# Optimization experiments

Hardware: AMD Instinct MI355X
Metric: run time of the kernel (lower is better)

## Reference

```python
import jax, jax.numpy as jnp
import numpy as np

B, S, H, HD = 8, 1024, 16, 64
D = H * HD
NINF = -10000.0
EPS = 1e-6


def setup_inputs() -> dict:
    key = jax.random.key(0)
    ks = jax.random.split(key, 6)
    std = 0.02
    return {
        "x": jax.random.normal(ks[0], (B, S, D), jnp.float32),
        "mask": jax.random.randint(ks[1], (B, S), 0, 2, jnp.int32),
        "wq": jax.random.normal(ks[2], (D, D), jnp.float32) * std,
        "bq": jnp.zeros((D,), jnp.float32),
        "wk": jax.random.normal(ks[3], (D, D), jnp.float32) * std,
        "bk": jnp.zeros((D,), jnp.float32),
        "wv": jax.random.normal(ks[4], (D, D), jnp.float32) * std,
        "bv": jnp.zeros((D,), jnp.float32),
        "wo": jax.random.normal(ks[5], (D, D), jnp.float32) * std,
        "bo": jnp.zeros((D,), jnp.float32),
        "gamma": jnp.ones((D,), jnp.float32),
        "beta": jnp.zeros((D,), jnp.float32),
    }


def _heads(t):
    # [B,S,D] -> [B,H,S,HD]
    return t.reshape(t.shape[0], t.shape[1], H, HD).transpose(0, 2, 1, 3)


def _layernorm(x, gamma, beta):
    mu = jnp.mean(x, -1, keepdims=True)
    var = jnp.mean(jnp.square(x - mu), -1, keepdims=True)
    return (x - mu) * jax.lax.rsqrt(var + EPS) * gamma + beta


def reference(x, mask, wq, bq, wk, bk, wv, bv, wo, bo, gamma, beta):
    q = _heads(x @ wq + bq)
    k = _heads(x @ wk + bk)
    v = _heads(x @ wv + bv)
    scores = jnp.einsum("bhqd,bhkd->bhqk", q, k) / np.sqrt(HD).astype(np.float32)
    # padding mask broadcast over key axis: 1 = masked
    scores = scores + mask.astype(jnp.float32)[:, None, None, :] * NINF
    attn = jax.nn.softmax(scores, axis=-1)
    ctx = jnp.einsum("bhqk,bhkd->bhqd", attn, v)  # [B,H,S,HD]
    ctx = ctx.transpose(0, 2, 1, 3).reshape(B, S, D)
    out = _layernorm(x + ctx @ wo + bo, gamma, beta)
    return out
```

## Files before the change

### kernel.cpp

```cpp
#include <hip/hip_runtime.h>
#include <stdint.h>

typedef unsigned short u16;
typedef unsigned int u32;
typedef __bf16 b16x8 __attribute__((ext_vector_type(8)));
typedef float f32x4 __attribute__((ext_vector_type(4)));

#define B_ 8
#define S_ 1024
#define H_ 16
#define HD_ 64
#define D_ 1024
#define M_ 8192

__device__ __forceinline__ u16 f2bf(float f) {
  u32 u = __float_as_uint(f);
  return (u16)((u + 0x7fffu + ((u >> 16) & 1u)) >> 16);
}
__device__ __forceinline__ u16 bfbits(float f) {
  union {
    __bf16 b;
    u16 u;
  } c;
  c.b = (__bf16)f;
  return c.u;
}

__device__ __forceinline__ f32x4 mfma16(b16x8 a, b16x8 b, f32x4 c) {
  return __builtin_amdgcn_mfma_f32_16x16x32_bf16(a, b, c, 0, 0, 0);
}

__device__ __forceinline__ void cp16(const u16* g, u16* l) {
  __builtin_amdgcn_global_load_lds(
      (const __attribute__((address_space(1))) u32*)(g),
      (__attribute__((address_space(3))) u32*)(l), 16, 0, 0);
}

__global__ __launch_bounds__(1024) void wconv_kernel(
    const float* __restrict__ w0, const float* __restrict__ w1,
    const float* __restrict__ w2, const float* __restrict__ w3,
    u16* __restrict__ t0, u16* __restrict__ t1, u16* __restrict__ t2,
    u16* __restrict__ t3) {
  __shared__ float tile[32][33];
  const int z = blockIdx.z;
  const float* src = (z == 0) ? w0 : (z == 1) ? w1 : (z == 2) ? w2 : w3;
  u16* dst = (z == 0) ? t0 : (z == 1) ? t1 : (z == 2) ? t2 : t3;
  const int tx = threadIdx.x, ty = threadIdx.y;
  const int x0 = blockIdx.x * 32, y0 = blockIdx.y * 32;
  tile[ty][tx] = src[(size_t)(y0 + ty) * D_ + x0 + tx];
  __syncthreads();
  dst[(size_t)(x0 + ty) * D_ + y0 + tx] = f2bf(tile[tx][ty]);
}

__global__ __launch_bounds__(256) void xconv_kernel(const float* __restrict__ x,
                                                    u16* __restrict__ xb) {
  const size_t i = ((size_t)blockIdx.x * 256 + threadIdx.x) * 4;
  const float4 v = *(const float4*)(x + i);
  u16 o[4] = {f2bf(v.x), f2bf(v.y), f2bf(v.z), f2bf(v.w)};
  uint2 pack;
  pack.x = ((u32)o[1] << 16) | o[0];
  pack.y = ((u32)o[3] << 16) | o[2];
  *(uint2*)(xb + i) = pack;
}

#define ABUF_ 16384
#define BBUF_ 8192
#define BUFSZ_ (ABUF_ + BBUF_)

__device__ __forceinline__ void gemm256x128_mainloop(
    const u16* __restrict__ A, const u16* __restrict__ BT, int K, int m0,
    int n0, u16* lds, f32x4 (&acc)[4][4]) {
  const int t = threadIdx.x;
  const int lane = t & 63;
  const int l15 = lane & 15;
  const int q4 = lane >> 4;
  const int w = t >> 6;
  const int wm = w >> 1;
  const int wn = w & 1;

  const f32x4 zero = {0.f, 0.f, 0.f, 0.f};
#pragma unroll
  for (int mt = 0; mt < 4; ++mt)
#pragma unroll
    for (int nt = 0; nt < 4; ++nt) acc[mt][nt] = zero;

  const int rbase = t >> 3;
  const int scol = ((t & 7) ^ (rbase & 7)) * 8;
  const u16* Ag = A + (size_t)(m0 + rbase) * K + scol;
  const u16* Bg = BT + (size_t)(n0 + rbase) * K + scol;
  const int sx = l15 & 7;

  auto STAGE = [&](int kt, int bufi) {
    u16* Ab = lds + bufi * BUFSZ_;
    u16* Bb = Ab + ABUF_;
    const int k0 = kt * 64;
#pragma unroll
    for (int c = 0; c < 4; ++c)
      cp16(Ag + (size_t)(c * 64) * K + k0, Ab + c * 4096 + t * 8);
#pragma unroll
    for (int c = 0; c < 2; ++c)
      cp16(Bg + (size_t)(c * 64) * K + k0, Bb + c * 4096 + t * 8);
  };

  const int NT = K / 64;
  STAGE(0, 0);
  STAGE(1, 1);

  int cur = 0;
  for (int kt = 0; kt < NT; ++kt) {
    if (kt + 2 < NT) {
      int nb = cur + 2;
      if (nb >= 3) nb -= 3;
      STAGE(kt + 2, nb);
    }
    if (kt + 2 < NT)
      asm volatile("s_waitcnt vmcnt(12)" ::: "memory");
    else if (kt + 1 < NT)
      asm volatile("s_waitcnt vmcnt(6)" ::: "memory");
    else
      asm volatile("s_waitcnt vmcnt(0)" ::: "memory");
    asm volatile("s_barrier" ::: "memory");

    const u16* Ab = lds + cur * BUFSZ_;
    const u16* Bb = Ab + ABUF_;

    b16x8 af[4][2], bf2[4][2];
#pragma unroll
    for (int kk = 0; kk < 2; ++kk) {
      const int cc = ((kk * 4 + q4) ^ sx) * 8;
#pragma unroll
      for (int mt = 0; mt < 4; ++mt)
        af[mt][kk] = *(const b16x8*)(Ab + (wm * 64 + mt * 16 + l15) * 64 + cc);
#pragma unroll
      for (int nt = 0; nt < 4; ++nt)
        bf2[nt][kk] = *(const b16x8*)(Bb + (wn * 64 + nt * 16 + l15) * 64 + cc);
    }
    __builtin_amdgcn_sched_barrier(0);

    __builtin_amdgcn_s_setprio(1);
#pragma unroll
    for (int mt = 0; mt < 4; ++mt)
#pragma unroll
      for (int nt = 0; nt < 4; ++nt)
        acc[mt][nt] = mfma16(af[mt][0], bf2[nt][0], acc[mt][nt]);
    __builtin_amdgcn_s_setprio(0);

    asm volatile("s_waitcnt lgkmcnt(0)" ::: "memory");
    asm volatile("s_barrier" ::: "memory");

    __builtin_amdgcn_s_setprio(1);
#pragma unroll
    for (int mt = 0; mt < 4; ++mt)
#pragma unroll
      for (int nt = 0; nt < 4; ++nt)
        acc[mt][nt] = mfma16(af[mt][1], bf2[nt][1], acc[mt][nt]);
    __builtin_amdgcn_s_setprio(0);

    ++cur;
    if (cur == 3) cur = 0;
  }
}

__global__ __launch_bounds__(512, 2) void qkv_gemm_kernel(
    const u16* __restrict__ xb, const u16* __restrict__ wt3,
    const float* __restrict__ bq, const float* __restrict__ bk,
    const float* __restrict__ bv, u16* __restrict__ Q, u16* __restrict__ Kb,
    u16* __restrict__ VT) {
  __shared__ __align__(16) u16 lds[3 * BUFSZ_];
  const int wg = blockIdx.x;
  const int xcd = wg & 7;
  const int s = wg >> 3;
  const int by = xcd * 4 + (s & 3);
  const int bx = s >> 2;
  const int m0 = by * 256;
  const int n0 = bx * 128;

  f32x4 acc[4][4];
  gemm256x128_mainloop(xb, wt3, D_, m0, n0, lds, acc);

  const int t = threadIdx.x;
  const int lane = t & 63, w = t >> 6;
  const int l15 = lane & 15, q4 = lane >> 4;
  const int wm = w >> 1, wn = w & 1;

  const int z = n0 >> 10;
  u16* out = (z == 0) ? Q : (z == 1) ? Kb : VT;
  const float* bias = (z == 0) ? bq : (z == 1) ? bk : bv;

  for (int nt = 0; nt < 4; ++nt) {
    const int nf = n0 + wn * 64 + nt * 16 + l15;
    const int n1 = nf & 1023;
    const float bias_v = bias[n1];
    const int h = n1 >> 6, hd = n1 & 63;
    for (int mt = 0; mt < 4; ++mt) {
      for (int r = 0; r < 4; ++r) {
        const int m = m0 + wm * 64 + mt * 16 + q4 * 4 + r;
        const int b = m >> 10, ss = m & 1023;
        const float v = acc[mt][nt][r] + bias_v;
        size_t idx;
        if (z < 2)
          idx = (((size_t)(b * H_ + h)) * S_ + ss) * HD_ + hd;
        else
          idx = (((size_t)(b * H_ + h)) * HD_ + hd) * S_ + ss;
        out[idx] = f2bf(v);
      }
    }
  }
}

#define PAD_ 68
#define QPAD_ 72
__global__ __launch_bounds__(512) void attn_kernel(
    const u16* __restrict__ Q, const u16* __restrict__ Kb,
    const u16* __restrict__ VT, const int* __restrict__ mask,
    u16* __restrict__ ctx) {
  __shared__ __align__(16) u16 QPlds[128 * QPAD_];
  __shared__ __align__(16) u16 Klds[64 * PAD_];
  __shared__ __align__(16) u16 Vlds[64 * PAD_];
  __shared__ __align__(16) float Mlds[1024];

  const int t = threadIdx.x;
  const int lane = t & 63, w = t >> 6;
  const int l15 = lane & 15, q4 = lane >> 4;
  const int id = blockIdx.x;
  const int bh = id & 127;
  const int b = bh >> 4, h = bh & 15;
  const int q0 = (id >> 7) * 128;

  const u16* Qbh = Q + (size_t)bh * S_ * HD_;
  const u16* Kbh = Kb + (size_t)bh * S_ * HD_;
  const u16* Vbh = VT + (size_t)bh * S_ * HD_;
  const int* maskb = mask + b * S_;

  const int srow = t >> 3, scol = (t & 7) * 8;
  {
    b16x8 q0v = *(const b16x8*)(Qbh + (size_t)(q0 + srow) * HD_ + scol);
    b16x8 q1v = *(const b16x8*)(Qbh + (size_t)(q0 + srow + 64) * HD_ + scol);
    const int2 mv = *(const int2*)(maskb + t * 2);
    *(b16x8*)(QPlds + srow * QPAD_ + scol) = q0v;
    *(b16x8*)(QPlds + (srow + 64) * QPAD_ + scol) = q1v;
    float2 mf;
    mf.x = -14427.0f * (float)mv.x;
    mf.y = -14427.0f * (float)mv.y;
    *(float2*)(Mlds + t * 2) = mf;
  }
  __syncthreads();
  b16x8 aq[2];
  aq[0] = *(const b16x8*)(QPlds + (w * 16 + l15) * QPAD_ + q4 * 8);
  aq[1] = *(const b16x8*)(QPlds + (w * 16 + l15) * QPAD_ + 32 + q4 * 8);

  const f32x4 zero = {0.f, 0.f, 0.f, 0.f};
  f32x4 acc[4];
  for (int nt = 0; nt < 4; ++nt) acc[nt] = zero;
  float lsum = 0.f;
  u16* Pw = QPlds + w * 16 * QPAD_;
  const float c1 = 0.18033688f;

  b16x8 kv0 = *(const b16x8*)(Kbh + (size_t)srow * HD_ + scol);
  b16x8 vv0 = *(const b16x8*)(Vbh + (size_t)srow * S_ + scol);

  for (int j = 0; j < 16; ++j) {
    const int key0 = j * 64;
    __syncthreads();
    *(b16x8*)(Klds + srow * PAD_ + scol) = kv0;
    *(b16x8*)(Vlds + srow * PAD_ + scol) = vv0;
    __syncthreads();

    if (j < 15) {
      const int kn = key0 + 64;
      kv0 = *(const b16x8*)(Kbh + (size_t)(kn + srow) * HD_ + scol);
      vv0 = *(const b16x8*)(Vbh + (size_t)srow * S_ + kn + scol);
    }

    f32x4 sf[4];
    for (int nt = 0; nt < 4; ++nt) sf[nt] = zero;
    for (int kk = 0; kk < 2; ++kk)
      for (int nt = 0; nt < 4; ++nt) {
        b16x8 bk =
            *(const b16x8*)(Klds + (nt * 16 + l15) * PAD_ + kk * 32 + q4 * 8);
        sf[nt] = mfma16(bk, aq[kk], sf[nt]);
      }

    for (int nt = 0; nt < 4; ++nt) {
      const float4 mk = *(const float4*)(Mlds + key0 + nt * 16 + q4 * 4);
      float p0 = __builtin_amdgcn_exp2f(sf[nt][0] * c1 + mk.x);
      float p1 = __builtin_amdgcn_exp2f(sf[nt][1] * c1 + mk.y);
      float p2 = __builtin_amdgcn_exp2f(sf[nt][2] * c1 + mk.z);
      float p3 = __builtin_amdgcn_exp2f(sf[nt][3] * c1 + mk.w);
      lsum += (p0 + p1) + (p2 + p3);
      uint2 pk;
      pk.x = ((u32)bfbits(p1) << 16) | bfbits(p0);
      pk.y = ((u32)bfbits(p3) << 16) | bfbits(p2);
      *(uint2*)(Pw + l15 * QPAD_ + nt * 16 + q4 * 4) = pk;
    }
    asm volatile("s_waitcnt lgkmcnt(0)" ::: "memory");

    for (int kk = 0; kk < 2; ++kk) {
      b16x8 bp = *(const b16x8*)(Pw + l15 * QPAD_ + kk * 32 + q4 * 8);
      for (int nt = 0; nt < 4; ++nt) {
        b16x8 vb =
            *(const b16x8*)(Vlds + (nt * 16 + l15) * PAD_ + kk * 32 + q4 * 8);
        acc[nt] = mfma16(vb, bp, acc[nt]);
      }
    }
  }

  lsum += __shfl_xor(lsum, 16);
  lsum += __shfl_xor(lsum, 32);
  const float inv = 1.0f / lsum;

  const int srw = q0 + w * 16 + l15;
  u16* crow = ctx + ((size_t)(b * S_ + srw)) * D_ + h * 64;
  for (int nt = 0; nt < 4; ++nt) {
    uint2 pk;
    pk.x = ((u32)bfbits(acc[nt][1] * inv) << 16) | bfbits(acc[nt][0] * inv);
    pk.y = ((u32)bfbits(acc[nt][3] * inv) << 16) | bfbits(acc[nt][2] * inv);
    *(uint2*)(crow + nt * 16 + q4 * 4) = pk;
  }
}

__global__ __launch_bounds__(512, 2) void out_gemm_kernel(
    const u16* __restrict__ ctx, const u16* __restrict__ wto,
    const float* __restrict__ bo, const float* __restrict__ x,
    float* __restrict__ y) {
  __shared__ __align__(16) u16 lds[3 * BUFSZ_];
  const int wg = blockIdx.x;
  const int xcd = wg & 7;
  const int s = wg >> 3;
  const int by = xcd * 4 + (s & 3);
  const int bx = s >> 2;
  const int m0 = by * 256, n0 = bx * 128;

  f32x4 acc[4][4];
  gemm256x128_mainloop(ctx, wto, D_, m0, n0, lds, acc);

  const int t = threadIdx.x;
  const int lane = t & 63, w = t >> 6;
  const int l15 = lane & 15, q4 = lane >> 4;
  const int wm = w >> 1, wn = w & 1;

  for (int nt = 0; nt < 4; ++nt) {
    const int n = n0 + wn * 64 + nt * 16 + l15;
    const float bias = bo[n];
    for (int mt = 0; mt < 4; ++mt) {
      for (int r = 0; r < 4; ++r) {
        const int m = m0 + wm * 64 + mt * 16 + q4 * 4 + r;
        y[(size_t)m * D_ + n] = acc[mt][nt][r] + bias + x[(size_t)m * D_ + n];
      }
    }
  }
}

__global__ __launch_bounds__(256) void ln_kernel(const float* __restrict__ y,
                                                 const float* __restrict__ g,
                                                 const float* __restrict__ be,
                                                 float* __restrict__ out) {
  const int row = blockIdx.x, t = threadIdx.x;
  const float* yr = y + (size_t)row * D_;
  const float4 v = *(const float4*)(yr + t * 4);
  float s = v.x + v.y + v.z + v.w;
  float ss = v.x * v.x + v.y * v.y + v.z * v.z + v.w * v.w;
  for (int off = 1; off < 64; off <<= 1) {
    s += __shfl_xor(s, off);
    ss += __shfl_xor(ss, off);
  }
  __shared__ float red[8];
  const int w = t >> 6, lane = t & 63;
  if (lane == 0) {
    red[w] = s;
    red[4 + w] = ss;
  }
  __syncthreads();
  s = red[0] + red[1] + red[2] + red[3];
  ss = red[4] + red[5] + red[6] + red[7];
  const float mu = s * (1.f / 1024.f);
  const float var = ss * (1.f / 1024.f) - mu * mu;
  const float rs = rsqrtf(var + 1e-6f);
  const int c = t * 4;
  const float4 gv = *(const float4*)(g + c);
  const float4 bv = *(const float4*)(be + c);
  float4 o;
  o.x = (v.x - mu) * rs * gv.x + bv.x;
  o.y = (v.y - mu) * rs * gv.y + bv.y;
  o.z = (v.z - mu) * rs * gv.z + bv.z;
  o.w = (v.w - mu) * rs * gv.w + bv.w;
  *(float4*)(out + (size_t)row * D_ + c) = o;
}

extern "C" void kernel_launch(void* const* d_in, const int* in_sizes, int n_in,
                              void* d_out, int out_size, void* d_ws,
                              size_t ws_size, hipStream_t stream) {
  const float* x = (const float*)d_in[0];
  const int* mask = (const int*)d_in[1];
  const float* wq = (const float*)d_in[2];
  const float* bq = (const float*)d_in[3];
  const float* wk = (const float*)d_in[4];
  const float* bk = (const float*)d_in[5];
  const float* wv = (const float*)d_in[6];
  const float* bv = (const float*)d_in[7];
  const float* wo = (const float*)d_in[8];
  const float* bo = (const float*)d_in[9];
  const float* gamma = (const float*)d_in[10];
  const float* beta = (const float*)d_in[11];
  float* out = (float*)d_out;

  char* ws = (char*)d_ws;
  const size_t MB = 1024ull * 1024ull;
  u16* wtq = (u16*)(ws + 0 * MB);
  u16* wtk = (u16*)(ws + 2 * MB);
  u16* wtv = (u16*)(ws + 4 * MB);
  u16* wto = (u16*)(ws + 6 * MB);
  u16* xb = (u16*)(ws + 8 * MB);
  u16* ctx = (u16*)(ws + 8 * MB);
  u16* Qb = (u16*)(ws + 24 * MB);
  u16* Kb = (u16*)(ws + 40 * MB);
  u16* VTb = (u16*)(ws + 56 * MB);
  float* y = (float*)(ws + 24 * MB);

  wconv_kernel<<<dim3(32, 32, 4), dim3(32, 32), 0, stream>>>(
      wq, wk, wv, wo, wtq, wtk, wtv, wto);
  xconv_kernel<<<8192, 256, 0, stream>>>(x, xb);
  qkv_gemm_kernel<<<768, 512, 0, stream>>>(xb, wtq, bq, bk, bv, Qb, Kb, VTb);
  attn_kernel<<<1024, 512, 0, stream>>>(Qb, Kb, VTb, mask, ctx);
  out_gemm_kernel<<<256, 512, 0, stream>>>(ctx, wto, bo, x, y);
  ln_kernel<<<8192, 256, 0, stream>>>(y, gamma, beta, out);
}
```

Measured before the change: 278.7 us.

## Shrink GEMM tiles to 128x128 with 256 threads and double buffering

```diff
diff --git a/kernel.cpp b/kernel.cpp
--- a/kernel.cpp
+++ b/kernel.cpp
@@ -63,11 +63,9 @@
   *(uint2*)(xb + i) = pack;
 }
 
-#define ABUF_ 16384
-#define BBUF_ 8192
-#define BUFSZ_ (ABUF_ + BBUF_)
-
-__device__ __forceinline__ void gemm256x128_mainloop(
+#define BUF128_ 16384
+
+__device__ __forceinline__ void gemm128_mainloop(
     const u16* __restrict__ A, const u16* __restrict__ BT, int K, int m0,
     int n0, u16* lds, f32x4 (&acc)[4][4]) {
   const int t = threadIdx.x;
@@ -75,8 +73,8 @@
   const int l15 = lane & 15;
   const int q4 = lane >> 4;
   const int w = t >> 6;
-  const int wm = w >> 1;
-  const int wn = w & 1;
+  const int mwave = (w >> 1) * 64;
+  const int nwave = (w & 1) * 64;
 
   const f32x4 zero = {0.f, 0.f, 0.f, 0.f};
 #pragma unroll
@@ -91,38 +89,31 @@
   const int sx = l15 & 7;
 
   auto STAGE = [&](int kt, int bufi) {
-    u16* Ab = lds + bufi * BUFSZ_;
-    u16* Bb = Ab + ABUF_;
+    u16* Ab = lds + bufi * BUF128_;
+    u16* Bb = Ab + 8192;
     const int k0 = kt * 64;
 #pragma unroll
     for (int c = 0; c < 4; ++c)
-      cp16(Ag + (size_t)(c * 64) * K + k0, Ab + c * 4096 + t * 8);
-#pragma unroll
-    for (int c = 0; c < 2; ++c)
-      cp16(Bg + (size_t)(c * 64) * K + k0, Bb + c * 4096 + t * 8);
+      cp16(Ag + (size_t)(c * 32) * K + k0, Ab + c * 2048 + t * 8);
+#pragma unroll
+    for (int c = 0; c < 4; ++c)
+      cp16(Bg + (size_t)(c * 32) * K + k0, Bb + c * 2048 + t * 8);
   };
 
   const int NT = K / 64;
   STAGE(0, 0);
-  STAGE(1, 1);
 
   int cur = 0;
   for (int kt = 0; kt < NT; ++kt) {
-    if (kt + 2 < NT) {
-      int nb = cur + 2;
-      if (nb >= 3) nb -= 3;
-      STAGE(kt + 2, nb);
-    }
-    if (kt + 2 < NT)
-      asm volatile("s_waitcnt vmcnt(12)" ::: "memory");
-    else if (kt + 1 < NT)
-      asm volatile("s_waitcnt vmcnt(6)" ::: "memory");
+    if (kt + 1 < NT) STAGE(kt + 1, cur ^ 1);
+    if (kt + 1 < NT)
+      asm volatile("s_waitcnt vmcnt(8)" ::: "memory");
     else
       asm volatile("s_waitcnt vmcnt(0)" ::: "memory");
     asm volatile("s_barrier" ::: "memory");
 
-    const u16* Ab = lds + cur * BUFSZ_;
-    const u16* Bb = Ab + ABUF_;
+    const u16* Ab = lds + cur * BUF128_;
+    const u16* Bb = Ab + 8192;
 
     b16x8 af[4][2], bf2[4][2];
 #pragma unroll
@@ -130,10 +121,10 @@
       const int cc = ((kk * 4 + q4) ^ sx) * 8;
 #pragma unroll
       for (int mt = 0; mt < 4; ++mt)
-        af[mt][kk] = *(const b16x8*)(Ab + (wm * 64 + mt * 16 + l15) * 64 + cc);
+        af[mt][kk] = *(const b16x8*)(Ab + (mwave + mt * 16 + l15) * 64 + cc);
 #pragma unroll
       for (int nt = 0; nt < 4; ++nt)
-        bf2[nt][kk] = *(const b16x8*)(Bb + (wn * 64 + nt * 16 + l15) * 64 + cc);
+        bf2[nt][kk] = *(const b16x8*)(Bb + (nwave + nt * 16 + l15) * 64 + cc);
     }
     __builtin_amdgcn_sched_barrier(0);
 
@@ -156,45 +147,44 @@
         acc[mt][nt] = mfma16(af[mt][1], bf2[nt][1], acc[mt][nt]);
     __builtin_amdgcn_s_setprio(0);
 
-    ++cur;
-    if (cur == 3) cur = 0;
-  }
-}
-
-__global__ __launch_bounds__(512, 2) void qkv_gemm_kernel(
+    cur ^= 1;
+  }
+}
+
+__global__ __launch_bounds__(256, 2) void qkv_gemm_kernel(
     const u16* __restrict__ xb, const u16* __restrict__ wt3,
     const float* __restrict__ bq, const float* __restrict__ bk,
     const float* __restrict__ bv, u16* __restrict__ Q, u16* __restrict__ Kb,
     u16* __restrict__ VT) {
-  __shared__ __align__(16) u16 lds[3 * BUFSZ_];
+  __shared__ __align__(16) u16 lds[2 * BUF128_];
   const int wg = blockIdx.x;
   const int xcd = wg & 7;
   const int s = wg >> 3;
-  const int by = xcd * 4 + (s & 3);
-  const int bx = s >> 2;
-  const int m0 = by * 256;
+  const int by = xcd * 8 + (s & 7);
+  const int bx = s >> 3;
+  const int m0 = by * 128;
   const int n0 = bx * 128;
 
   f32x4 acc[4][4];
-  gemm256x128_mainloop(xb, wt3, D_, m0, n0, lds, acc);
+  gemm128_mainloop(xb, wt3, D_, m0, n0, lds, acc);
 
   const int t = threadIdx.x;
   const int lane = t & 63, w = t >> 6;
   const int l15 = lane & 15, q4 = lane >> 4;
-  const int wm = w >> 1, wn = w & 1;
+  const int mwave = (w >> 1) * 64, nwave = (w & 1) * 64;
 
   const int z = n0 >> 10;
   u16* out = (z == 0) ? Q : (z == 1) ? Kb : VT;
   const float* bias = (z == 0) ? bq : (z == 1) ? bk : bv;
 
   for (int nt = 0; nt < 4; ++nt) {
-    const int nf = n0 + wn * 64 + nt * 16 + l15;
+    const int nf = n0 + nwave + nt * 16 + l15;
     const int n1 = nf & 1023;
     const float bias_v = bias[n1];
     const int h = n1 >> 6, hd = n1 & 63;
     for (int mt = 0; mt < 4; ++mt) {
       for (int r = 0; r < 4; ++r) {
-        const int m = m0 + wm * 64 + mt * 16 + q4 * 4 + r;
+        const int m = m0 + mwave + mt * 16 + q4 * 4 + r;
         const int b = m >> 10, ss = m & 1023;
         const float v = acc[mt][nt][r] + bias_v;
         size_t idx;
@@ -319,32 +309,32 @@
   }
 }
 
-__global__ __launch_bounds__(512, 2) void out_gemm_kernel(
+__global__ __launch_bounds__(256, 2) void out_gemm_kernel(
     const u16* __restrict__ ctx, const u16* __restrict__ wto,
     const float* __restrict__ bo, const float* __restrict__ x,
     float* __restrict__ y) {
-  __shared__ __align__(16) u16 lds[3 * BUFSZ_];
+  __shared__ __align__(16) u16 lds[2 * BUF128_];
   const int wg = blockIdx.x;
   const int xcd = wg & 7;
   const int s = wg >> 3;
-  const int by = xcd * 4 + (s & 3);
-  const int bx = s >> 2;
-  const int m0 = by * 256, n0 = bx * 128;
+  const int by = xcd * 8 + (s & 7);
+  const int bx = s >> 3;
+  const int m0 = by * 128, n0 = bx * 128;
 
   f32x4 acc[4][4];
-  gemm256x128_mainloop(ctx, wto, D_, m0, n0, lds, acc);
+  gemm128_mainloop(ctx, wto, D_, m0, n0, lds, acc);
 
   const int t = threadIdx.x;
   const int lane = t & 63, w = t >> 6;
   const int l15 = lane & 15, q4 = lane >> 4;
-  const int wm = w >> 1, wn = w & 1;
+  const int mwave = (w >> 1) * 64, nwave = (w & 1) * 64;
 
   for (int nt = 0; nt < 4; ++nt) {
-    const int n = n0 + wn * 64 + nt * 16 + l15;
+    const int n = n0 + nwave + nt * 16 + l15;
     const float bias = bo[n];
     for (int mt = 0; mt < 4; ++mt) {
       for (int r = 0; r < 4; ++r) {
-        const int m = m0 + wm * 64 + mt * 16 + q4 * 4 + r;
+        const int m = m0 + mwave + mt * 16 + q4 * 4 + r;
         y[(size_t)m * D_ + n] = acc[mt][nt][r] + bias + x[(size_t)m * D_ + n];
       }
     }
@@ -420,8 +410,8 @@
   wconv_kernel<<<dim3(32, 32, 4), dim3(32, 32), 0, stream>>>(
       wq, wk, wv, wo, wtq, wtk, wtv, wto);
   xconv_kernel<<<8192, 256, 0, stream>>>(x, xb);
-  qkv_gemm_kernel<<<768, 512, 0, stream>>>(xb, wtq, bq, bk, bv, Qb, Kb, VTb);
+  qkv_gemm_kernel<<<1536, 256, 0, stream>>>(xb, wtq, bq, bk, bv, Qb, Kb, VTb);
   attn_kernel<<<1024, 512, 0, stream>>>(Qb, Kb, VTb, mask, ctx);
-  out_gemm_kernel<<<256, 512, 0, stream>>>(ctx, wto, bo, x, y);
+  out_gemm_kernel<<<512, 256, 0, stream>>>(ctx, wto, bo, x, y);
   ln_kernel<<<8192, 256, 0, stream>>>(y, gamma, beta, out);
 }
```

Result: no change. 280.8 us (+0.8%).

## Use 128x128 double-buffered QKV GEMM tiles and 128-key attention blocks

Applied to the files above, without the earlier changes.

```diff
diff --git a/kernel.cpp b/kernel.cpp
--- a/kernel.cpp
+++ b/kernel.cpp
@@ -63,6 +63,141 @@
   *(uint2*)(xb + i) = pack;
 }
 
+#define BUF128_ 16384
+
+__device__ __forceinline__ void gemm128_mainloop(
+    const u16* __restrict__ A, const u16* __restrict__ BT, int K, int m0,
+    int n0, u16* lds, f32x4 (&acc)[4][4]) {
+  const int t = threadIdx.x;
+  const int lane = t & 63;
+  const int l15 = lane & 15;
+  const int q4 = lane >> 4;
+  const int w = t >> 6;
+  const int mwave = (w >> 1) * 64;
+  const int nwave = (w & 1) * 64;
+
+  const f32x4 zero = {0.f, 0.f, 0.f, 0.f};
+#pragma unroll
+  for (int mt = 0; mt < 4; ++mt)
+#pragma unroll
+    for (int nt = 0; nt < 4; ++nt) acc[mt][nt] = zero;
+
+  const int rbase = t >> 3;
+  const int scol = ((t & 7) ^ (rbase & 7)) * 8;
+  const u16* Ag = A + (size_t)(m0 + rbase) * K + scol;
+  const u16* Bg = BT + (size_t)(n0 + rbase) * K + scol;
+  const int sx = l15 & 7;
+
+  auto STAGE = [&](int kt, int bufi) {
+    u16* Ab = lds + bufi * BUF128_;
+    u16* Bb = Ab + 8192;
+    const int k0 = kt * 64;
+#pragma unroll
+    for (int c = 0; c < 4; ++c)
+      cp16(Ag + (size_t)(c * 32) * K + k0, Ab + c * 2048 + t * 8);
+#pragma unroll
+    for (int c = 0; c < 4; ++c)
+      cp16(Bg + (size_t)(c * 32) * K + k0, Bb + c * 2048 + t * 8);
+  };
+
+  const int NT = K / 64;
+  STAGE(0, 0);
+
+  int cur = 0;
+  for (int kt = 0; kt < NT; ++kt) {
+    if (kt + 1 < NT) STAGE(kt + 1, cur ^ 1);
+    if (kt + 1 < NT)
+      asm volatile("s_waitcnt vmcnt(8)" ::: "memory");
+    else
+      asm volatile("s_waitcnt vmcnt(0)" ::: "memory");
+    asm volatile("s_barrier" ::: "memory");
+
+    const u16* Ab = lds + cur * BUF128_;
+    const u16* Bb = Ab + 8192;
+
+    b16x8 af[4][2], bf2[4][2];
+#pragma unroll
+    for (int kk = 0; kk < 2; ++kk) {
+      const int cc = ((kk * 4 + q4) ^ sx) * 8;
+#pragma unroll
+      for (int mt = 0; mt < 4; ++mt)
+        af[mt][kk] = *(const b16x8*)(Ab + (mwave + mt * 16 + l15) * 64 + cc);
+#pragma unroll
+      for (int nt = 0; nt < 4; ++nt)
+        bf2[nt][kk] = *(const b16x8*)(Bb + (nwave + nt * 16 + l15) * 64 + cc);
+    }
+    __builtin_amdgcn_sched_barrier(0);
+
+    __builtin_amdgcn_s_setprio(1);
+#pragma unroll
+    for (int mt = 0; mt < 4; ++mt)
+#pragma unroll
+      for (int nt = 0; nt < 4; ++nt)
+        acc[mt][nt] = mfma16(af[mt][0], bf2[nt][0], acc[mt][nt]);
+    __builtin_amdgcn_s_setprio(0);
+
+    asm volatile("s_waitcnt lgkmcnt(0)" ::: "memory");
+    asm volatile("s_barrier" ::: "memory");
+
+    __builtin_amdgcn_s_setprio(1);
+#pragma unroll
+    for (int mt = 0; mt < 4; ++mt)
+#pragma unroll
+      for (int nt = 0; nt < 4; ++nt)
+        acc[mt][nt] = mfma16(af[mt][1], bf2[nt][1], acc[mt][nt]);
+    __builtin_amdgcn_s_setprio(0);
+
+    cur ^= 1;
+  }
+}
+
+__global__ __launch_bounds__(256, 2) void qkv_gemm_kernel(
+    const u16* __restrict__ xb, const u16* __restrict__ wt3,
+    const float* __restrict__ bq, const float* __restrict__ bk,
+    const float* __restrict__ bv, u16* __restrict__ Q, u16* __restrict__ Kb,
+    u16* __restrict__ VT) {
+  __shared__ __align__(16) u16 lds[2 * BUF128_];
+  const int wg = blockIdx.x;
+  const int xcd = wg & 7;
+  const int s = wg >> 3;
+  const int by = xcd * 8 + (s & 7);
+  const int bx = s >> 3;
+  const int m0 = by * 128;
+  const int n0 = bx * 128;
+
+  f32x4 acc[4][4];
+  gemm128_mainloop(xb, wt3, D_, m0, n0, lds, acc);
+
+  const int t = threadIdx.x;
+  const int lane = t & 63, w = t >> 6;
+  const int l15 = lane & 15, q4 = lane >> 4;
+  const int mwave = (w >> 1) * 64, nwave = (w & 1) * 64;
+
+  const int z = n0 >> 10;
+  u16* out = (z == 0) ? Q : (z == 1) ? Kb : VT;
+  const float* bias = (z == 0) ? bq : (z == 1) ? bk : bv;
+
+  for (int nt = 0; nt < 4; ++nt) {
+    const int nf = n0 + nwave + nt * 16 + l15;
+    const int n1 = nf & 1023;
+    const float bias_v = bias[n1];
+    const int h = n1 >> 6, hd = n1 & 63;
+    for (int mt = 0; mt < 4; ++mt) {
+      for (int r = 0; r < 4; ++r) {
+        const int m = m0 + mwave + mt * 16 + q4 * 4 + r;
+        const int b = m >> 10, ss = m & 1023;
+        const float v = acc[mt][nt][r] + bias_v;
+        size_t idx;
+        if (z < 2)
+          idx = (((size_t)(b * H_ + h)) * S_ + ss) * HD_ + hd;
+        else
+          idx = (((size_t)(b * H_ + h)) * HD_ + hd) * S_ + ss;
+        out[idx] = f2bf(v);
+      }
+    }
+  }
+}
+
 #define ABUF_ 16384
 #define BBUF_ 8192
 #define BUFSZ_ (ABUF_ + BBUF_)
@@ -161,62 +296,16 @@
   }
 }
 
-__global__ __launch_bounds__(512, 2) void qkv_gemm_kernel(
-    const u16* __restrict__ xb, const u16* __restrict__ wt3,
-    const float* __restrict__ bq, const float* __restrict__ bk,
-    const float* __restrict__ bv, u16* __restrict__ Q, u16* __restrict__ Kb,
-    u16* __restrict__ VT) {
-  __shared__ __align__(16) u16 lds[3 * BUFSZ_];
-  const int wg = blockIdx.x;
-  const int xcd = wg & 7;
-  const int s = wg >> 3;
-  const int by = xcd * 4 + (s & 3);
-  const int bx = s >> 2;
-  const int m0 = by * 256;
-  const int n0 = bx * 128;
-
-  f32x4 acc[4][4];
-  gemm256x128_mainloop(xb, wt3, D_, m0, n0, lds, acc);
-
-  const int t = threadIdx.x;
-  const int lane = t & 63, w = t >> 6;
-  const int l15 = lane & 15, q4 = lane >> 4;
-  const int wm = w >> 1, wn = w & 1;
-
-  const int z = n0 >> 10;
-  u16* out = (z == 0) ? Q : (z == 1) ? Kb : VT;
-  const float* bias = (z == 0) ? bq : (z == 1) ? bk : bv;
-
-  for (int nt = 0; nt < 4; ++nt) {
-    const int nf = n0 + wn * 64 + nt * 16 + l15;
-    const int n1 = nf & 1023;
-    const float bias_v = bias[n1];
-    const int h = n1 >> 6, hd = n1 & 63;
-    for (int mt = 0; mt < 4; ++mt) {
-      for (int r = 0; r < 4; ++r) {
-        const int m = m0 + wm * 64 + mt * 16 + q4 * 4 + r;
-        const int b = m >> 10, ss = m & 1023;
-        const float v = acc[mt][nt][r] + bias_v;
-        size_t idx;
-        if (z < 2)
-          idx = (((size_t)(b * H_ + h)) * S_ + ss) * HD_ + hd;
-        else
-          idx = (((size_t)(b * H_ + h)) * HD_ + hd) * S_ + ss;
-        out[idx] = f2bf(v);
-      }
-    }
-  }
-}
-
 #define PAD_ 68
+#define VPAD_ 136
 #define QPAD_ 72
 __global__ __launch_bounds__(512) void attn_kernel(
     const u16* __restrict__ Q, const u16* __restrict__ Kb,
     const u16* __restrict__ VT, const int* __restrict__ mask,
     u16* __restrict__ ctx) {
   __shared__ __align__(16) u16 QPlds[128 * QPAD_];
-  __shared__ __align__(16) u16 Klds[64 * PAD_];
-  __shared__ __align__(16) u16 Vlds[64 * PAD_];
+  __shared__ __align__(16) u16 Klds[128 * PAD_];
+  __shared__ __align__(16) u16 Vlds[64 * VPAD_];
   __shared__ __align__(16) float Mlds[1024];
 
   const int t = threadIdx.x;
@@ -257,50 +346,60 @@
   const float c1 = 0.18033688f;
 
   b16x8 kv0 = *(const b16x8*)(Kbh + (size_t)srow * HD_ + scol);
+  b16x8 kv1 = *(const b16x8*)(Kbh + (size_t)(srow + 64) * HD_ + scol);
   b16x8 vv0 = *(const b16x8*)(Vbh + (size_t)srow * S_ + scol);
-
-  for (int j = 0; j < 16; ++j) {
-    const int key0 = j * 64;
+  b16x8 vv1 = *(const b16x8*)(Vbh + (size_t)srow * S_ + 64 + scol);
+
+  for (int j = 0; j < 8; ++j) {
+    const int key0 = j * 128;
     __syncthreads();
     *(b16x8*)(Klds + srow * PAD_ + scol) = kv0;
-    *(b16x8*)(Vlds + srow * PAD_ + scol) = vv0;
+    *(b16x8*)(Klds + (srow + 64) * PAD_ + scol) = kv1;
+    *(b16x8*)(Vlds + srow * VPAD_ + scol) = vv0;
+    *(b16x8*)(Vlds + srow * VPAD_ + 64 + scol) = vv1;
     __syncthreads();
 
-    if (j < 15) {
-      const int kn = key0 + 64;
+    if (j < 7) {
+      const int kn = key0 + 128;
       kv0 = *(const b16x8*)(Kbh + (size_t)(kn + srow) * HD_ + scol);
+      kv1 = *(const b16x8*)(Kbh + (size_t)(kn + srow + 64) * HD_ + scol);
       vv0 = *(const b16x8*)(Vbh + (size_t)srow * S_ + kn + scol);
-    }
-
-    f32x4 sf[4];
-    for (int nt = 0; nt < 4; ++nt) sf[nt] = zero;
-    for (int kk = 0; kk < 2; ++kk)
+      vv1 = *(const b16x8*)(Vbh + (size_t)srow * S_ + kn + 64 + scol);
+    }
+
+#pragma unroll
+    for (int ks = 0; ks < 2; ++ks) {
+      f32x4 sf[4];
+      for (int nt = 0; nt < 4; ++nt) sf[nt] = zero;
+      for (int kk = 0; kk < 2; ++kk)
+        for (int nt = 0; nt < 4; ++nt) {
+          b16x8 bk = *(const b16x8*)(Klds + (ks * 64 + nt * 16 + l15) * PAD_ +
+                                     kk * 32 + q4 * 8);
+          sf[nt] = mfma16(bk, aq[kk], sf[nt]);
+        }
+
       for (int nt = 0; nt < 4; ++nt) {
-        b16x8 bk =
-            *(const b16x8*)(Klds + (nt * 16 + l15) * PAD_ + kk * 32 + q4 * 8);
-        sf[nt] = mfma16(bk, aq[kk], sf[nt]);
+        const float4 mk =
+            *(const float4*)(Mlds + key0 + ks * 64 + nt * 16 + q4 * 4);
+        float p0 = __builtin_amdgcn_exp2f(sf[nt][0] * c1 + mk.x);
+        float p1 = __builtin_amdgcn_exp2f(sf[nt][1] * c1 + mk.y);
+        float p2 = __builtin_amdgcn_exp2f(sf[nt][2] * c1 + mk.z);
+        float p3 = __builtin_amdgcn_exp2f(sf[nt][3] * c1 + mk.w);
+        lsum += (p0 + p1) + (p2 + p3);
+        uint2 pk;
+        pk.x = ((u32)bfbits(p1) << 16) | bfbits(p0);
+        pk.y = ((u32)bfbits(p3) << 16) | bfbits(p2);
+        *(uint2*)(Pw + l15 * QPAD_ + nt * 16 + q4 * 4) = pk;
       }
-
-    for (int nt = 0; nt < 4; ++nt) {
-      const float4 mk = *(const float4*)(Mlds + key0 + nt * 16 + q4 * 4);
-      float p0 = __builtin_amdgcn_exp2f(sf[nt][0] * c1 + mk.x);
-      float p1 = __builtin_amdgcn_exp2f(sf[nt][1] * c1 + mk.y);
-      float p2 = __builtin_amdgcn_exp2f(sf[nt][2] * c1 + mk.z);
-      float p3 = __builtin_amdgcn_exp2f(sf[nt][3] * c1 + mk.w);
-      lsum += (p0 + p1) + (p2 + p3);
-      uint2 pk;
-      pk.x = ((u32)bfbits(p1) << 16) | bfbits(p0);
-      pk.y = ((u32)bfbits(p3) << 16) | bfbits(p2);
-      *(uint2*)(Pw + l15 * QPAD_ + nt * 16 + q4 * 4) = pk;
-    }
-    asm volatile("s_waitcnt lgkmcnt(0)" ::: "memory");
-
-    for (int kk = 0; kk < 2; ++kk) {
-      b16x8 bp = *(const b16x8*)(Pw + l15 * QPAD_ + kk * 32 + q4 * 8);
-      for (int nt = 0; nt < 4; ++nt) {
-        b16x8 vb =
-            *(const b16x8*)(Vlds + (nt * 16 + l15) * PAD_ + kk * 32 + q4 * 8);
-        acc[nt] = mfma16(vb, bp, acc[nt]);
+      asm volatile("s_waitcnt lgkmcnt(0)" ::: "memory");
+
+      for (int kk = 0; kk < 2; ++kk) {
+        b16x8 bp = *(const b16x8*)(Pw + l15 * QPAD_ + kk * 32 + q4 * 8);
+        for (int nt = 0; nt < 4; ++nt) {
+          b16x8 vb = *(const b16x8*)(Vlds + (nt * 16 + l15) * VPAD_ + ks * 64 +
+                                     kk * 32 + q4 * 8);
+          acc[nt] = mfma16(vb, bp, acc[nt]);
+        }
       }
     }
   }
@@ -420,7 +519,7 @@
   wconv_kernel<<<dim3(32, 32, 4), dim3(32, 32), 0, stream>>>(
       wq, wk, wv, wo, wtq, wtk, wtv, wto);
   xconv_kernel<<<8192, 256, 0, stream>>>(x, xb);
-  qkv_gemm_kernel<<<768, 512, 0, stream>>>(xb, wtq, bq, bk, bv, Qb, Kb, VTb);
+  qkv_gemm_kernel<<<1536, 256, 0, stream>>>(xb, wtq, bq, bk, bv, Qb, Kb, VTb);
   attn_kernel<<<1024, 512, 0, stream>>>(Qb, Kb, VTb, mask, ctx);
   out_gemm_kernel<<<256, 512, 0, stream>>>(ctx, wto, bo, x, y);
   ln_kernel<<<8192, 256, 0, stream>>>(y, gamma, beta, out);
```

Measured after the change: 273.2 us. -2.0%, faster.
